# Kernel optimization log

Measured on AMD Instinct MI355X. Metric: run time of the kernel, lower is better.

The kernel has to match this reference:

```python
import jax, jax.numpy as jnp
import numpy as np

DIM = 4096
N_HEADS = 32
N_KV_HEADS = 8
HEAD_DIM = 128
ROPE_THETA = 10000.0
REPEATS = N_HEADS // N_KV_HEADS
SCALE = HEAD_DIM ** -0.5


def rope(x, seq_len, offset):
    # x: [b, h, seq_len, head_dim]; faithful to source: cos/sin from cat((freqs,freqs)),
    # rotate built by interleaved pair swap then flatten.
    d = x.shape[-1]
    inv_freq = 1.0 / (ROPE_THETA ** (jnp.arange(0, d, 2, dtype=jnp.float32) / d))  # [d/2]
    t = jnp.arange(offset, offset + seq_len, dtype=jnp.float32)                    # [L]
    freqs = t[:, None] * inv_freq[None, :]                                         # [L, d/2]
    emb = jnp.concatenate([freqs, freqs], axis=-1)                                 # [L, d]
    cos_emb = jnp.cos(emb)
    sin_emb = jnp.sin(emb)
    x_even = x[..., 0::2]
    x_odd = x[..., 1::2]
    rotate_x = jnp.stack([-x_odd, x_even], axis=-1).reshape(x.shape)
    return x * cos_emb + rotate_x * sin_emb


def setup_inputs() -> dict:
    key = jax.random.key(0)
    k1, k2, k3, k4, k5 = jax.random.split(key, 5)
    b, l = 1, 2048
    s = 0.02
    x = jax.random.normal(k1, (b, l, DIM), dtype=jnp.float32)
    wq = jax.random.normal(k2, (DIM, N_HEADS * HEAD_DIM), dtype=jnp.float32) * s
    wk = jax.random.normal(k3, (DIM, N_KV_HEADS * HEAD_DIM), dtype=jnp.float32) * s
    wv = jax.random.normal(k4, (DIM, N_KV_HEADS * HEAD_DIM), dtype=jnp.float32) * s
    wo = jax.random.normal(k5, (N_HEADS * HEAD_DIM, DIM), dtype=jnp.float32) * s
    return {"x": x, "wq": wq, "wk": wk, "wv": wv, "wo": wo, "seq_len": l}


def reference(x, wq, wk, wv, wo, seq_len):
    b, l, _ = x.shape
    q = (x @ wq).reshape(b, l, N_HEADS, HEAD_DIM).transpose(0, 2, 1, 3)       # [b,H,l,d]
    k = (x @ wk).reshape(b, l, N_KV_HEADS, HEAD_DIM).transpose(0, 2, 1, 3)    # [b,Hk,l,d]
    v = (x @ wv).reshape(b, l, N_KV_HEADS, HEAD_DIM).transpose(0, 2, 1, 3)
    # repeat KV heads to match query heads (GQA)
    k = jnp.repeat(k, REPEATS, axis=1)   # [b,H,l,d]
    v = jnp.repeat(v, REPEATS, axis=1)
    offset = 0  # cache is None
    q = rope(q, seq_len, offset)
    k = rope(k, seq_len, offset)
    scores = jnp.einsum('bhid,bhjd->bhij', q * SCALE, k)
    scores = jax.nn.softmax(scores.astype(jnp.float32), axis=-1).astype(scores.dtype)
    out = jnp.einsum('bhij,bhjd->bhid', scores, v)
    out = out.transpose(0, 2, 1, 3).reshape(b, l, N_HEADS * HEAD_DIM)
    return out @ wo, (k, v)
```

## Files before the change

kernel.cpp:

```cpp
#include <hip/hip_runtime.h>
#include <cstdint>
#include <cstddef>

#define DIM 4096
#define SEQ 2048
#define NH 32
#define NKV 8
#define HD 128
#define QKVN 6144

typedef __bf16 bf16_t;
typedef __bf16 bf16x8 __attribute__((ext_vector_type(8)));
typedef __bf16 bf16x4 __attribute__((ext_vector_type(4)));
typedef __bf16 bf16x2 __attribute__((ext_vector_type(2)));
typedef float f32x4 __attribute__((ext_vector_type(4)));
typedef int int4v __attribute__((ext_vector_type(4)));

__device__ __forceinline__ f32x4 mfma16(bf16x8 a, bf16x8 b, f32x4 c) {
  return __builtin_amdgcn_mfma_f32_16x16x32_bf16(a, b, c, 0, 0, 0);
}

__device__ __forceinline__ void async16(const bf16_t* g, bf16_t* l) {
  __builtin_amdgcn_global_load_lds((__attribute__((address_space(1))) void*)g,
                                   (__attribute__((address_space(3))) void*)l,
                                   16, 0, 0);
}

__device__ __forceinline__ int pack2(float a, float b) {
  bf16x2 h = { (bf16_t)a, (bf16_t)b };
  return __builtin_bit_cast(int, h);
}

__global__ void cast_x(const float* __restrict__ x, bf16_t* __restrict__ xb) {
  int i = blockIdx.x * 256 + threadIdx.x;
  const float4 v = ((const float4*)x)[i];
  bf16x4 o = { (bf16_t)v.x, (bf16_t)v.y, (bf16_t)v.z, (bf16_t)v.w };
  *(bf16x4*)(xb + (size_t)i * 4) = o;
}

__global__ void tcast(const float* __restrict__ src, bf16_t* __restrict__ dst,
                      int Ncols, int Kdim) {
  __shared__ float tile[32][33];
  int n0 = blockIdx.x * 32, k0 = blockIdx.y * 32;
  int tx = threadIdx.x, ty = threadIdx.y;
#pragma unroll
  for (int r = 0; r < 4; r++)
    tile[ty + 8 * r][tx] = src[(size_t)(k0 + ty + 8 * r) * Ncols + n0 + tx];
  __syncthreads();
#pragma unroll
  for (int r = 0; r < 4; r++)
    dst[(size_t)(n0 + ty + 8 * r) * Kdim + k0 + tx] = (bf16_t)tile[tx][ty + 8 * r];
}

__global__ __launch_bounds__(256) void gemm_bt(const bf16_t* __restrict__ A,
                                               const bf16_t* __restrict__ Bt,
                                               float* __restrict__ C,
                                               int M, int N, int K) {
  __shared__ bf16_t As[128 * 32];
  __shared__ bf16_t Bs[128 * 32];
  const int t = threadIdx.x;
  const int bm = blockIdx.y * 128, bn = blockIdx.x * 128;
  const int lane = t & 63, l15 = lane & 15, quad = lane >> 4;
  const int w = t >> 6;
  const int wm = (w & 1) * 64, wn = (w >> 1) * 64;
  f32x4 acc[4][4] = {};
  const bf16_t* gA = A + (size_t)(bm + (t >> 2)) * K + (t & 3) * 8;
  const bf16_t* gB = Bt + (size_t)(bn + (t >> 2)) * K + (t & 3) * 8;
  bf16_t* lA = As + t * 8;
  bf16_t* lB = Bs + t * 8;
  for (int k0 = 0; k0 < K; k0 += 32) {
    async16(gA + k0, lA);
    async16(gA + k0 + (size_t)64 * K, lA + 2048);
    async16(gB + k0, lB);
    async16(gB + k0 + (size_t)64 * K, lB + 2048);
    __syncthreads();
    bf16x8 af[4], bfr[4];
#pragma unroll
    for (int mi = 0; mi < 4; mi++)
      af[mi] = *(const bf16x8*)(As + (wm + mi * 16 + l15) * 32 + quad * 8);
#pragma unroll
    for (int ni = 0; ni < 4; ni++)
      bfr[ni] = *(const bf16x8*)(Bs + (wn + ni * 16 + l15) * 32 + quad * 8);
#pragma unroll
    for (int mi = 0; mi < 4; mi++)
#pragma unroll
      for (int ni = 0; ni < 4; ni++)
        acc[mi][ni] = mfma16(af[mi], bfr[ni], acc[mi][ni]);
    __syncthreads();
  }
#pragma unroll
  for (int mi = 0; mi < 4; mi++)
#pragma unroll
    for (int ni = 0; ni < 4; ni++) {
      size_t row = (size_t)bm + wm + mi * 16 + quad * 4;
      size_t col = (size_t)bn + wn + ni * 16 + l15;
#pragma unroll
      for (int r = 0; r < 4; r++)
        C[(row + r) * N + col] = acc[mi][ni][r];
    }
}

__global__ void rope_scatter(const float* __restrict__ qkv, bf16_t* __restrict__ Qb,
                             bf16_t* __restrict__ Kb, bf16_t* __restrict__ Vt,
                             float* __restrict__ kOut, float* __restrict__ vOut) {
  int idx = blockIdx.x * 256 + threadIdx.x;
  int t = idx / 3072;
  int p = idx - t * 3072;
  const float NEG_L2T_64 = -0.20762050593046f;
  const float SS = 0.08838834764831845f * 1.4426950408889634f;
  if (p < 2048) {
    int hh = p >> 6, pr = p & 63;
    int d0 = pr << 1;
    const float* src = qkv + (size_t)t * QKVN + hh * HD + d0;
    float a = src[0], b = src[1];
    int j0 = d0 & 63, j1 = (d0 + 1) & 63;
    float th0 = (float)t * exp2f((float)j0 * NEG_L2T_64);
    float th1 = (float)t * exp2f((float)j1 * NEG_L2T_64);
    float o0 = (a * cosf(th0) - b * sinf(th0)) * SS;
    float o1 = (b * cosf(th1) + a * sinf(th1)) * SS;
    bf16_t* dst = Qb + ((size_t)hh * SEQ + t) * HD + d0;
    dst[0] = (bf16_t)o0;
    dst[1] = (bf16_t)o1;
  } else if (p < 2560) {
    int q2 = p - 2048;
    int kh = q2 >> 6, pr = q2 & 63;
    int d0 = pr << 1;
    const float* src = qkv + (size_t)t * QKVN + 4096 + kh * HD + d0;
    float a = src[0], b = src[1];
    int j0 = d0 & 63, j1 = (d0 + 1) & 63;
    float th0 = (float)t * exp2f((float)j0 * NEG_L2T_64);
    float th1 = (float)t * exp2f((float)j1 * NEG_L2T_64);
    float o0 = a * cosf(th0) - b * sinf(th0);
    float o1 = b * cosf(th1) + a * sinf(th1);
    bf16_t* dst = Kb + ((size_t)kh * SEQ + t) * HD + d0;
    dst[0] = (bf16_t)o0;
    dst[1] = (bf16_t)o1;
#pragma unroll
    for (int rep = 0; rep < 4; rep++) {
      float* kp = kOut + ((size_t)(kh * 4 + rep) * SEQ + t) * HD + d0;
      kp[0] = o0;
      kp[1] = o1;
    }
  } else {
    int q2 = p - 2560;
    int kh = q2 >> 6, pr = q2 & 63;
    int d0 = pr << 1;
    const float* src = qkv + (size_t)t * QKVN + 5120 + kh * HD + d0;
    float a = src[0], b = src[1];
#pragma unroll
    for (int rep = 0; rep < 4; rep++) {
      float* vp = vOut + ((size_t)(kh * 4 + rep) * SEQ + t) * HD + d0;
      vp[0] = a;
      vp[1] = b;
    }
    int tp = (t & ~31) + ((t & 12) << 1) + (t & 3) + ((t & 16) >> 2);
    Vt[((size_t)kh * HD + d0) * SEQ + tp] = (bf16_t)a;
    Vt[((size_t)kh * HD + d0 + 1) * SEQ + tp] = (bf16_t)b;
  }
}

__global__ __launch_bounds__(512, 2) void attn_kernel(const bf16_t* __restrict__ Qb,
                                                      const bf16_t* __restrict__ Kb,
                                                      const bf16_t* __restrict__ Vt,
                                                      bf16_t* __restrict__ AO) {
  __shared__ bf16_t Ks[2][8192];
  __shared__ bf16_t Vs[2][8192];
  const int h = blockIdx.y, kh = h >> 2;
  const int qbase = blockIdx.x * 256;
  const int w = threadIdx.x >> 6, lane = threadIdx.x & 63;
  const int l15 = lane & 15, quad = lane >> 4;
  const bf16_t* KbH = Kb + (size_t)kh * SEQ * HD;
  const bf16_t* VtH = Vt + (size_t)kh * HD * SEQ;

  bf16x8 qf[2][4];
#pragma unroll
  for (int nq = 0; nq < 2; nq++) {
    const bf16_t* qp = Qb + ((size_t)h * SEQ + qbase + w * 32 + nq * 16 + l15) * HD + quad * 8;
#pragma unroll
    for (int kc = 0; kc < 4; kc++) qf[nq][kc] = *(const bf16x8*)(qp + kc * 32);
  }

  f32x4 acc[8][2] = {};
  float rsum[2] = {0.f, 0.f};

  auto stage = [&](int buf, int kt0) {
    if (w < 4) {
      int kc = w;
#pragma unroll
      for (int kg = 0; kg < 4; kg++) {
        const bf16_t* g = KbH + (size_t)(kt0 + kg * 16 + (lane >> 2)) * HD + kc * 32 + (lane & 3) * 8;
        async16(g, &Ks[buf][kc * 2048 + kg * 512]);
      }
    } else {
      int vi = w - 4, kt = vi >> 1, dg0 = (vi & 1) * 4;
#pragma unroll
      for (int j = 0; j < 4; j++) {
        int dg = dg0 + j;
        const bf16_t* g = VtH + (size_t)(dg * 16 + (lane >> 2)) * SEQ + kt0 + kt * 32 + (lane & 3) * 8;
        async16(g, &Vs[buf][kt * 4096 + dg * 512]);
      }
    }
  };

  stage(0, 0);
  int buf = 0;

  for (int kt0 = 0; kt0 < SEQ; kt0 += 64, buf ^= 1) {
    __syncthreads();
    if (kt0 + 64 < SEQ) stage(buf ^ 1, kt0 + 64);

    f32x4 sacc[4][2] = {};
#pragma unroll
    for (int mi = 0; mi < 4; mi++)
#pragma unroll
      for (int kc = 0; kc < 4; kc++) {
        bf16x8 kf = *(const bf16x8*)(&Ks[buf][(kc * 64 + mi * 16 + l15) * 32 + quad * 8]);
#pragma unroll
        for (int nq = 0; nq < 2; nq++)
          sacc[mi][nq] = mfma16(kf, qf[nq][kc], sacc[mi][nq]);
      }

    int pk[4][2][2];
#pragma unroll
    for (int mi = 0; mi < 4; mi++)
#pragma unroll
      for (int nq = 0; nq < 2; nq++) {
        float p0 = exp2f(sacc[mi][nq][0]);
        float p1 = exp2f(sacc[mi][nq][1]);
        float p2 = exp2f(sacc[mi][nq][2]);
        float p3 = exp2f(sacc[mi][nq][3]);
        rsum[nq] += (p0 + p1) + (p2 + p3);
        pk[mi][nq][0] = pack2(p0, p1);
        pk[mi][nq][1] = pack2(p2, p3);
      }

#pragma unroll
    for (int kt = 0; kt < 2; kt++) {
#pragma unroll
      for (int nq = 0; nq < 2; nq++) {
        int4v dw;
        dw[0] = pk[2 * kt][nq][0];
        dw[1] = pk[2 * kt][nq][1];
        dw[2] = pk[2 * kt + 1][nq][0];
        dw[3] = pk[2 * kt + 1][nq][1];
        bf16x8 pf = __builtin_bit_cast(bf16x8, dw);
#pragma unroll
        for (int dt = 0; dt < 8; dt++) {
          bf16x8 vf = *(const bf16x8*)(&Vs[buf][(kt * 128 + dt * 16 + l15) * 32 + quad * 8]);
          acc[dt][nq] = mfma16(vf, pf, acc[dt][nq]);
        }
      }
    }
  }

#pragma unroll
  for (int nq = 0; nq < 2; nq++) {
    float rs = rsum[nq];
    rs += __shfl_xor(rs, 16);
    rs += __shfl_xor(rs, 32);
    float inv = 1.0f / rs;
    int q = qbase + w * 32 + nq * 16 + l15;
#pragma unroll
    for (int dt = 0; dt < 8; dt++) {
      bf16x4 o = { (bf16_t)(acc[dt][nq][0] * inv), (bf16_t)(acc[dt][nq][1] * inv),
                   (bf16_t)(acc[dt][nq][2] * inv), (bf16_t)(acc[dt][nq][3] * inv) };
      *(bf16x4*)(AO + (size_t)q * DIM + h * HD + dt * 16 + quad * 4) = o;
    }
  }
}

extern "C" void kernel_launch(void* const* d_in, const int* in_sizes, int n_in,
                              void* d_out, int out_size, void* d_ws, size_t ws_size,
                              hipStream_t stream) {
  const float* x = (const float*)d_in[0];
  const float* wq = (const float*)d_in[1];
  const float* wk = (const float*)d_in[2];
  const float* wv = (const float*)d_in[3];
  const float* wo = (const float*)d_in[4];
  float* out = (float*)d_out;
  float* kOut = out + (size_t)SEQ * DIM;
  float* vOut = kOut + (size_t)NH * SEQ * HD;

  char* ws = (char*)d_ws;
  bf16_t* Xb = (bf16_t*)ws;
  bf16_t* WT = (bf16_t*)(ws + 16777216);
  float* QKV = (float*)(ws + 67108864);
  bf16_t* WoT = (bf16_t*)(ws + 67108864);
  bf16_t* Qb = (bf16_t*)(ws + 117440512);
  bf16_t* Kb = (bf16_t*)(ws + 134217728);
  bf16_t* Vt = (bf16_t*)(ws + 138412032);
  bf16_t* AO = Xb;

  dim3 tb(32, 8);
  cast_x<<<8192, 256, 0, stream>>>(x, Xb);
  tcast<<<dim3(128, 128), tb, 0, stream>>>(wq, WT, 4096, 4096);
  tcast<<<dim3(32, 128), tb, 0, stream>>>(wk, WT + (size_t)4096 * 4096, 1024, 4096);
  tcast<<<dim3(32, 128), tb, 0, stream>>>(wv, WT + (size_t)5120 * 4096, 1024, 4096);
  gemm_bt<<<dim3(48, 16), 256, 0, stream>>>(Xb, WT, QKV, 2048, 6144, 4096);
  rope_scatter<<<24576, 256, 0, stream>>>(QKV, Qb, Kb, Vt, kOut, vOut);
  tcast<<<dim3(128, 128), tb, 0, stream>>>(wo, WoT, 4096, 4096);
  attn_kernel<<<dim3(8, 32), 512, 0, stream>>>(Qb, Kb, Vt, AO);
  gemm_bt<<<dim3(32, 16), 256, 0, stream>>>(AO, WoT, out, 2048, 4096, 4096);
}
```

Baseline: 595.9 us.

## Replace GEMM with 256x256 double-buffered, swizzled, prioritized MFMA kernel

Replaces the 128x128 single-buffered GEMM with a 256x256-tile, 512-thread kernel. It uses a K=64 step, double-buffered LDS with async global-to-LDS prefetch overlapped with the MFMAs, an XOR-swizzled LDS layout to avoid bank conflicts, a workgroup-ID remap for L2 locality, and s_setprio around the MFMA bursts. The aim is to raise arithmetic intensity and hide load latency in both projection GEMMs. In exchange it uses 128KB of LDS and many barriers, and the grids shrink to 192 and 128 workgroups, which may underfill the 256 CUs.

```diff
diff --git a/kernel.cpp b/kernel.cpp
--- a/kernel.cpp
+++ b/kernel.cpp
@@ -31,6 +31,10 @@
   return __builtin_bit_cast(int, h);
 }
 
+#define LGKM0() do { asm volatile("s_waitcnt lgkmcnt(0)" ::: "memory"); \
+                     __builtin_amdgcn_sched_barrier(0); } while (0)
+#define VM0() do { asm volatile("s_waitcnt vmcnt(0)" ::: "memory"); } while (0)
+
 __global__ void cast_x(const float* __restrict__ x, bf16_t* __restrict__ xb) {
   int i = blockIdx.x * 256 + threadIdx.x;
   const float4 v = ((const float4*)x)[i];
@@ -52,48 +56,153 @@
     dst[(size_t)(n0 + ty + 8 * r) * Kdim + k0 + tx] = (bf16_t)tile[tx][ty + 8 * r];
 }
 
-__global__ __launch_bounds__(256) void gemm_bt(const bf16_t* __restrict__ A,
+__global__ __launch_bounds__(512) void gemm256(const bf16_t* __restrict__ A,
                                                const bf16_t* __restrict__ Bt,
                                                float* __restrict__ C,
                                                int M, int N, int K) {
-  __shared__ bf16_t As[128 * 32];
-  __shared__ bf16_t Bs[128 * 32];
+  __shared__ bf16_t As[2][16384];
+  __shared__ bf16_t Bs[2][16384];
   const int t = threadIdx.x;
-  const int bm = blockIdx.y * 128, bn = blockIdx.x * 128;
-  const int lane = t & 63, l15 = lane & 15, quad = lane >> 4;
-  const int w = t >> 6;
-  const int wm = (w & 1) * 64, wn = (w >> 1) * 64;
-  f32x4 acc[4][4] = {};
-  const bf16_t* gA = A + (size_t)(bm + (t >> 2)) * K + (t & 3) * 8;
-  const bf16_t* gB = Bt + (size_t)(bn + (t >> 2)) * K + (t & 3) * 8;
-  bf16_t* lA = As + t * 8;
-  bf16_t* lB = Bs + t * 8;
-  for (int k0 = 0; k0 < K; k0 += 32) {
-    async16(gA + k0, lA);
-    async16(gA + k0 + (size_t)64 * K, lA + 2048);
-    async16(gB + k0, lB);
-    async16(gB + k0 + (size_t)64 * K, lB + 2048);
-    __syncthreads();
-    bf16x8 af[4], bfr[4];
-#pragma unroll
-    for (int mi = 0; mi < 4; mi++)
-      af[mi] = *(const bf16x8*)(As + (wm + mi * 16 + l15) * 32 + quad * 8);
-#pragma unroll
-    for (int ni = 0; ni < 4; ni++)
-      bfr[ni] = *(const bf16x8*)(Bs + (wn + ni * 16 + l15) * 32 + quad * 8);
-#pragma unroll
-    for (int mi = 0; mi < 4; mi++)
-#pragma unroll
-      for (int ni = 0; ni < 4; ni++)
-        acc[mi][ni] = mfma16(af[mi], bfr[ni], acc[mi][ni]);
-    __syncthreads();
+  const int lane = t & 63;
+  const int l15 = lane & 15, quad = lane >> 4;
+  const int w = t >> 6, wm = w >> 2, wn = w & 3;
+
+  const int gx = gridDim.x;
+  const int nwg = gx * gridDim.y;
+  const int id = blockIdx.y * gx + blockIdx.x;
+  const int swz = (id & 7) * (nwg >> 3) + (id >> 3);
+  const int bm = (swz / gx) * 256, bn = (swz % gx) * 256;
+
+  const int srow = t >> 3;
+  const int scol = ((t & 7) << 3) ^ ((t >> 1) & 16);
+  const bf16_t* gA = A + (size_t)(bm + srow) * K + scol;
+  const bf16_t* gB = Bt + (size_t)(bn + srow) * K + scol;
+  const int ldst = t * 8;
+
+  const int qx = (quad * 8) ^ ((l15 & 4) ? 16 : 0);
+  const int aBase = wm * 8192 + l15 * 64 + qx;
+  const int bBase = (wn >> 1) * 8192 + ((wn & 1) * 64 + l15) * 64 + qx;
+
+  f32x4 acc[8][4] = {};
+  bf16x8 af[4][2], bfr[2][2];
+
+#pragma unroll
+  for (int h = 0; h < 2; h++)
+#pragma unroll
+    for (int i = 0; i < 2; i++) {
+      async16(gA + (size_t)(h * 128 + i * 64) * K, &As[0][h * 8192 + i * 4096 + ldst]);
+      async16(gB + (size_t)(h * 128 + i * 64) * K, &Bs[0][h * 8192 + i * 4096 + ldst]);
+    }
+  VM0();
+  __builtin_amdgcn_s_barrier();
+
+  const int nkt = K >> 6;
+  for (int kt = 0; kt < nkt; ++kt) {
+    const int buf = kt & 1;
+    const int k1 = (kt + 1) << 6;
+    const bool pf = (kt + 1) < nkt;
+
+#pragma unroll
+    for (int mi = 0; mi < 4; mi++)
+#pragma unroll
+      for (int s = 0; s < 2; s++)
+        af[mi][s] = *(const bf16x8*)&As[buf][aBase + mi * 1024 + s * 32];
+#pragma unroll
+    for (int ni = 0; ni < 2; ni++)
+#pragma unroll
+      for (int s = 0; s < 2; s++)
+        bfr[ni][s] = *(const bf16x8*)&Bs[buf][bBase + ni * 1024 + s * 32];
+    if (pf) {
+#pragma unroll
+      for (int h = 0; h < 2; h++)
+#pragma unroll
+        for (int i = 0; i < 2; i++)
+          async16(gA + (size_t)(h * 128 + i * 64) * K + k1,
+                  &As[buf ^ 1][h * 8192 + i * 4096 + ldst]);
+    }
+    __builtin_amdgcn_s_barrier();
+    LGKM0();
+    __builtin_amdgcn_s_setprio(1);
+#pragma unroll
+    for (int mi = 0; mi < 4; mi++)
+#pragma unroll
+      for (int ni = 0; ni < 2; ni++)
+#pragma unroll
+        for (int s = 0; s < 2; s++)
+          acc[mi][ni] = mfma16(af[mi][s], bfr[ni][s], acc[mi][ni]);
+    __builtin_amdgcn_s_setprio(0);
+    __builtin_amdgcn_s_barrier();
+
+#pragma unroll
+    for (int ni = 0; ni < 2; ni++)
+#pragma unroll
+      for (int s = 0; s < 2; s++)
+        bfr[ni][s] = *(const bf16x8*)&Bs[buf][bBase + (ni + 2) * 1024 + s * 32];
+    if (pf) {
+#pragma unroll
+      for (int h = 0; h < 2; h++)
+#pragma unroll
+        for (int i = 0; i < 2; i++)
+          async16(gB + (size_t)(h * 128 + i * 64) * K + k1,
+                  &Bs[buf ^ 1][h * 8192 + i * 4096 + ldst]);
+    }
+    __builtin_amdgcn_s_barrier();
+    LGKM0();
+    __builtin_amdgcn_s_setprio(1);
+#pragma unroll
+    for (int mi = 0; mi < 4; mi++)
+#pragma unroll
+      for (int ni = 0; ni < 2; ni++)
+#pragma unroll
+        for (int s = 0; s < 2; s++)
+          acc[mi][ni + 2] = mfma16(af[mi][s], bfr[ni][s], acc[mi][ni + 2]);
+    __builtin_amdgcn_s_setprio(0);
+    __builtin_amdgcn_s_barrier();
+
+#pragma unroll
+    for (int mi = 0; mi < 4; mi++)
+#pragma unroll
+      for (int s = 0; s < 2; s++)
+        af[mi][s] = *(const bf16x8*)&As[buf][aBase + (mi + 4) * 1024 + s * 32];
+    __builtin_amdgcn_s_barrier();
+    LGKM0();
+    __builtin_amdgcn_s_setprio(1);
+#pragma unroll
+    for (int mi = 0; mi < 4; mi++)
+#pragma unroll
+      for (int ni = 0; ni < 2; ni++)
+#pragma unroll
+        for (int s = 0; s < 2; s++)
+          acc[mi + 4][ni + 2] = mfma16(af[mi][s], bfr[ni][s], acc[mi + 4][ni + 2]);
+    __builtin_amdgcn_s_setprio(0);
+    __builtin_amdgcn_s_barrier();
+
+#pragma unroll
+    for (int ni = 0; ni < 2; ni++)
+#pragma unroll
+      for (int s = 0; s < 2; s++)
+        bfr[ni][s] = *(const bf16x8*)&Bs[buf][bBase + ni * 1024 + s * 32];
+    __builtin_amdgcn_s_barrier();
+    LGKM0();
+    __builtin_amdgcn_s_setprio(1);
+#pragma unroll
+    for (int mi = 0; mi < 4; mi++)
+#pragma unroll
+      for (int ni = 0; ni < 2; ni++)
+#pragma unroll
+        for (int s = 0; s < 2; s++)
+          acc[mi + 4][ni] = mfma16(af[mi][s], bfr[ni][s], acc[mi + 4][ni]);
+    __builtin_amdgcn_s_setprio(0);
+    VM0();
+    __builtin_amdgcn_s_barrier();
   }
-#pragma unroll
-  for (int mi = 0; mi < 4; mi++)
+
+#pragma unroll
+  for (int mi = 0; mi < 8; mi++)
 #pragma unroll
     for (int ni = 0; ni < 4; ni++) {
-      size_t row = (size_t)bm + wm + mi * 16 + quad * 4;
-      size_t col = (size_t)bn + wn + ni * 16 + l15;
+      size_t row = (size_t)bm + wm * 128 + mi * 16 + quad * 4;
+      size_t col = (size_t)bn + wn * 64 + ni * 16 + l15;
 #pragma unroll
       for (int r = 0; r < 4; r++)
         C[(row + r) * N + col] = acc[mi][ni][r];
@@ -296,9 +405,9 @@
   tcast<<<dim3(128, 128), tb, 0, stream>>>(wq, WT, 4096, 4096);
   tcast<<<dim3(32, 128), tb, 0, stream>>>(wk, WT + (size_t)4096 * 4096, 1024, 4096);
   tcast<<<dim3(32, 128), tb, 0, stream>>>(wv, WT + (size_t)5120 * 4096, 1024, 4096);
-  gemm_bt<<<dim3(48, 16), 256, 0, stream>>>(Xb, WT, QKV, 2048, 6144, 4096);
+  gemm256<<<dim3(24, 8), 512, 0, stream>>>(Xb, WT, QKV, 2048, 6144, 4096);
   rope_scatter<<<24576, 256, 0, stream>>>(QKV, Qb, Kb, Vt, kOut, vOut);
   tcast<<<dim3(128, 128), tb, 0, stream>>>(wo, WoT, 4096, 4096);
   attn_kernel<<<dim3(8, 32), 512, 0, stream>>>(Qb, Kb, Vt, AO);
-  gemm_bt<<<dim3(32, 16), 256, 0, stream>>>(AO, WoT, out, 2048, 4096, 4096);
-}
+  gemm256<<<dim3(16, 8), 512, 0, stream>>>(AO, WoT, out, 2048, 4096, 4096);
+}
```

After: 607.5 us. About the same (+1.9%).
